# Optimization experiments

Hardware: AMD Instinct MI355X
Metric: run time of the kernel (lower is better)

## Reference

```python
import jax, jax.numpy as jnp
import numpy as np

TOP_K = 2
LORA_SCALE = 32.0 / 16.0  # alpha / r


def setup_inputs() -> dict:
    key = jax.random.key(0)
    ks = jax.random.split(key, 11)
    B, S, H, I, E, R = 4, 2048, 2048, 5504, 8, 16
    s = lambda k, shape, fan: jax.random.normal(k, shape, jnp.float32) / np.sqrt(fan)
    return {
        "x": jax.random.normal(ks[0], (B, S, H), jnp.float32),
        "gate_values": jax.random.normal(ks[1], (B, E), jnp.float32),
        "Wg": s(ks[2], (I, H), H),
        "Ag": s(ks[3], (E, H, R), H),
        "Bg": s(ks[4], (E, R, I), R),
        "Wu": s(ks[5], (I, H), H),
        "Au": s(ks[6], (E, H, R), H),
        "Bu": s(ks[7], (E, R, I), R),
        "Wd": s(ks[8], (H, I), I),
        "Ad": s(ks[9], (E, I, R), I),
        "Bd": s(ks[10], (E, R, H), R),
    }


def _top_k_binary_gates(gate_values, k):
    # set top-k entries per row to 1.0, others 0.0 (bsz, num_experts)
    _, idx = jax.lax.top_k(gate_values, k)
    b = jnp.zeros_like(gate_values)
    rows = jnp.arange(gate_values.shape[0])[:, None]
    return b.at[rows, idx].set(1.0)


def _adapter_linear(x, W, A, B, binary_gates):
    # base: (b,s,in) @ (out,in)^T -> (b,s,out)
    base = jnp.einsum("bsh,oh->bso", x, W)
    # per-expert LoRA: gate e * x @ A_e @ B_e, summed over selected experts
    u = jnp.einsum("bsh,ehr->bser", x, A)            # (b,s,E,r) low-rank
    delta = jnp.einsum("bser,ero,be->bso", u, B, binary_gates)
    return base + LORA_SCALE * delta


def reference(x, gate_values, Wg, Ag, Bg, Wu, Au, Bu, Wd, Ad, Bd):
    g = _top_k_binary_gates(gate_values, TOP_K)
    gate_out = _adapter_linear(x, Wg, Ag, Bg, g)
    up_out = _adapter_linear(x, Wu, Au, Bu, g)
    h = jax.nn.silu(gate_out) * up_out              # SwiGLU
    return _adapter_linear(h, Wd, Ad, Bd, g)
```

## Files before the change

### kernel.cpp

```cpp
#include <hip/hip_runtime.h>
#include <stdint.h>

typedef unsigned short u16;
typedef __bf16 bf16x8 __attribute__((ext_vector_type(8)));
typedef float f32x4 __attribute__((ext_vector_type(4)));

#define AS1 __attribute__((address_space(1)))
#define AS3 __attribute__((address_space(3)))

__device__ __forceinline__ void g2l16(const void* g, void* l) {
  __builtin_amdgcn_global_load_lds((AS1 void*)(void*)g, (AS3 void*)l, 16, 0, 0);
}

__device__ __forceinline__ u16 f2bf(float f) {
  union { float f; uint32_t u; } v; v.f = f;
  return (u16)((v.u + 0x7fffu + ((v.u >> 16) & 1u)) >> 16);
}
__device__ __forceinline__ float bf2f(u16 b) {
  union { uint32_t u; float f; } v; v.u = ((uint32_t)b) << 16;
  return v.f;
}

__global__ void k_cast4(const float* __restrict__ x, u16* __restrict__ xb,
                        const float* __restrict__ Wg, u16* __restrict__ Wgb,
                        const float* __restrict__ Wu, u16* __restrict__ Wub,
                        const float* __restrict__ Wd, u16* __restrict__ Wdb) {
  int i = blockIdx.x * 256 + threadIdx.x;
  const float* in; u16* out; int j;
  if (i < 4194304) { in = x; out = xb; j = i; }
  else if (i < 4194304 + 2818048) { in = Wg; out = Wgb; j = i - 4194304; }
  else if (i < 4194304 + 2 * 2818048) { in = Wu; out = Wub; j = i - 4194304 - 2818048; }
  else { in = Wd; out = Wdb; j = i - 4194304 - 2 * 2818048; }
  float4 v = ((const float4*)in)[j];
  ushort4 o = make_ushort4(f2bf(v.x), f2bf(v.y), f2bf(v.z), f2bf(v.w));
  ((ushort4*)out)[j] = o;
}

__global__ void k_prep(const float* __restrict__ gv,
                       const float* __restrict__ Ag, const float* __restrict__ Au,
                       const float* __restrict__ Ad,
                       const float* __restrict__ Bg, const float* __restrict__ Bu,
                       const float* __restrict__ Bd,
                       u16* __restrict__ AxT, u16* __restrict__ AdT,
                       u16* __restrict__ BgT, u16* __restrict__ BuT,
                       u16* __restrict__ BdT) {
  __shared__ int sidx[8];
  if (threadIdx.x == 0) {
    #pragma unroll
    for (int b = 0; b < 4; ++b) {
      const float* g = gv + b * 8;
      int i1 = 0; float v1 = g[0];
      for (int e = 1; e < 8; ++e) if (g[e] > v1) { v1 = g[e]; i1 = e; }
      int i2 = -1; float v2 = -3.0e38f;
      for (int e = 0; e < 8; ++e) if (e != i1 && g[e] > v2) { v2 = g[e]; i2 = e; }
      sidx[2 * b] = i1; sidx[2 * b + 1] = i2;
    }
  }
  __syncthreads();
  int t = blockIdx.x * 256 + threadIdx.x;
  if (t < 524288) {
    int h = t % 2048;
    int j = (t / 2048) & 63;
    int b = t / (2048 * 64);
    const float* src = (j >= 32) ? Au : Ag;
    int jj = j & 31;
    int e = sidx[2 * b + ((jj >> 4) & 1)];
    AxT[t] = f2bf(src[((size_t)e * 2048 + h) * 16 + (jj & 15)]);
    return;
  }
  t -= 524288;
  if (t < 704512) {
    int h = t % 5504;
    int j = (t / 5504) & 31;
    int b = t / (5504 * 32);
    int e = sidx[2 * b + ((j >> 4) & 1)];
    AdT[t] = f2bf(Ad[((size_t)e * 5504 + h) * 16 + (j & 15)]);
    return;
  }
  t -= 704512;
  if (t < 704512) {
    int j = t & 31;
    int n = (t >> 5) % 5504;
    int b = t / (5504 * 32);
    int e = (j & 16) ? sidx[2 * b + 1] : sidx[2 * b];
    BgT[t] = f2bf(Bg[((size_t)e * 16 + (j & 15)) * 5504 + n]);
    return;
  }
  t -= 704512;
  if (t < 704512) {
    int j = t & 31;
    int n = (t >> 5) % 5504;
    int b = t / (5504 * 32);
    int e = (j & 16) ? sidx[2 * b + 1] : sidx[2 * b];
    BuT[t] = f2bf(Bu[((size_t)e * 16 + (j & 15)) * 5504 + n]);
    return;
  }
  t -= 704512;
  if (t < 262144) {
    int j = t & 31;
    int n = (t >> 5) % 2048;
    int b = t / (2048 * 32);
    int e = (j & 16) ? sidx[2 * b + 1] : sidx[2 * b];
    BdT[t] = f2bf(Bd[((size_t)e * 16 + (j & 15)) * 2048 + n]);
  }
}

template <int N2>
__global__ __launch_bounds__(256) void k_skinny(
    const u16* __restrict__ A, const u16* __restrict__ BT,
    float* __restrict__ part, int M, int K, int total_iters, int iters_per_chunk) {
  __shared__ u16 sA[128 * 64];
  __shared__ u16 sB[N2 * 64];
  int nm = M >> 7;
  int bm = blockIdx.x % nm, chunk = blockIdx.x / nm;
  int m0 = bm << 7;
  int batch = m0 >> 11;
  int tid = threadIdx.x, lane = tid & 63, w = tid >> 6;
  int kb = chunk * iters_per_chunk;
  int ke = min(total_iters, kb + iters_per_chunk);

  const u16* Bb = BT + (size_t)batch * N2 * K;

  const u16* ga[4]; u16* la[4];
  #pragma unroll
  for (int t = 0; t < 4; ++t) {
    int cb = 4 * w + t;
    int q = cb * 64 + lane;
    int row = q >> 3;
    int c = (q & 7) ^ (row & 7);
    ga[t] = A + (size_t)(m0 + row) * K + (size_t)kb * 64 + c * 8;
    la[t] = sA + cb * 512;
  }
  constexpr int nB = N2 / 32;
  const u16* gb[nB]; u16* lb[nB];
  #pragma unroll
  for (int t = 0; t < nB; ++t) {
    int cb = nB * w + t;
    int q = cb * 64 + lane;
    int row = q >> 3;
    int c = (q & 7) ^ (row & 7);
    gb[t] = Bb + (size_t)row * K + (size_t)kb * 64 + c * 8;
    lb[t] = sB + cb * 512;
  }

  f32x4 acc[2][N2 / 16] = {};
  for (int kt = kb; kt < ke; ++kt) {
    #pragma unroll
    for (int t = 0; t < 4; ++t) { g2l16(ga[t], la[t]); ga[t] += 64; }
    #pragma unroll
    for (int t = 0; t < nB; ++t) { g2l16(gb[t], lb[t]); gb[t] += 64; }
    __syncthreads();
    #pragma unroll
    for (int ks = 0; ks < 2; ++ks) {
      int cb0 = ks * 4 + (lane >> 4);
      bf16x8 af[2], bfr[N2 / 16];
      #pragma unroll
      for (int mi = 0; mi < 2; ++mi) {
        int row = 32 * w + mi * 16 + (lane & 15);
        af[mi] = *(const bf16x8*)(sA + (row * 8 + (cb0 ^ (row & 7))) * 8);
      }
      #pragma unroll
      for (int ni = 0; ni < N2 / 16; ++ni) {
        int row = ni * 16 + (lane & 15);
        bfr[ni] = *(const bf16x8*)(sB + (row * 8 + (cb0 ^ (row & 7))) * 8);
      }
      #pragma unroll
      for (int mi = 0; mi < 2; ++mi)
        #pragma unroll
        for (int ni = 0; ni < N2 / 16; ++ni)
          acc[mi][ni] = __builtin_amdgcn_mfma_f32_16x16x32_bf16(
              af[mi], bfr[ni], acc[mi][ni], 0, 0, 0);
    }
    __syncthreads();
  }

  int rb = (lane >> 4) * 4, cc = lane & 15;
  #pragma unroll
  for (int mi = 0; mi < 2; ++mi)
    #pragma unroll
    for (int ni = 0; ni < N2 / 16; ++ni)
      #pragma unroll
      for (int reg = 0; reg < 4; ++reg) {
        int gr = m0 + 32 * w + mi * 16 + rb + reg;
        int gc = ni * 16 + cc;
        part[((size_t)chunk * M + gr) * N2 + gc] = acc[mi][ni][reg];
      }
}

__global__ void k_fin(const float* __restrict__ part, u16* __restrict__ out0,
                      u16* __restrict__ out1, int M, int N2, int nch) {
  int t = blockIdx.x * 256 + threadIdx.x;
  if (t >= M * N2) return;
  float s = 0.f;
  for (int c = 0; c < nch; ++c) s += part[(size_t)c * M * N2 + t];
  int j = t % N2, bs = t / N2;
  u16 v = f2bf(2.0f * s);
  if (N2 == 64) {
    if (j < 32) out0[(size_t)bs * 32 + j] = v;
    else        out1[(size_t)bs * 32 + (j - 32)] = v;
  } else {
    out0[(size_t)bs * 32 + j] = v;
  }
}

__global__ __launch_bounds__(256, 2)
void k_gemmGU(const u16* __restrict__ A, const u16* __restrict__ Bg_,
              const u16* __restrict__ Bu_,
              const u16* __restrict__ A2g, const u16* __restrict__ A2u,
              const u16* __restrict__ B2g, const u16* __restrict__ B2u,
              u16* __restrict__ Out, int N, int K) {
  __shared__ u16 sA[128 * 64];
  __shared__ u16 sG[128 * 64];
  __shared__ u16 sU[128 * 64];
  int nt = N >> 7;
  int nm = gridDim.x / nt;
  int perx = nm >> 3;
  int xcd = blockIdx.x & 7;
  int v = blockIdx.x >> 3;
  int bn = v / perx;
  int bm = xcd * perx + (v - bn * perx);
  int m0 = bm << 7, n0 = bn << 7;
  int tid = threadIdx.x, lane = tid & 63, w = tid >> 6;
  int mo = (w & 1) << 6, no = (w >> 1) << 6;

  const u16* ga[4]; const u16* gg[4]; const u16* gu[4];
  u16* la[4]; u16* lg[4]; u16* lu[4];
  #pragma unroll
  for (int t = 0; t < 4; ++t) {
    int cb = 4 * w + t;
    int q = cb * 64 + lane;
    int row = q >> 3;
    int c = (q & 7) ^ (row & 7);
    ga[t] = A + (size_t)(m0 + row) * K + c * 8;
    gg[t] = Bg_ + (size_t)(n0 + row) * K + c * 8;
    gu[t] = Bu_ + (size_t)(n0 + row) * K + c * 8;
    la[t] = sA + cb * 512;
    lg[t] = sG + cb * 512;
    lu[t] = sU + cb * 512;
  }

  f32x4 accg[4][4] = {};
  f32x4 accu[4][4] = {};

  int kiters = K >> 6;
  for (int kt = 0; kt < kiters; ++kt) {
    #pragma unroll
    for (int t = 0; t < 4; ++t) { g2l16(ga[t], la[t]); ga[t] += 64; }
    #pragma unroll
    for (int t = 0; t < 4; ++t) { g2l16(gg[t], lg[t]); gg[t] += 64; }
    #pragma unroll
    for (int t = 0; t < 4; ++t) { g2l16(gu[t], lu[t]); gu[t] += 64; }
    __syncthreads();
    #pragma unroll
    for (int ks = 0; ks < 2; ++ks) {
      bf16x8 af[4], bgf[4], buf_[4];
      int cb0 = ks * 4 + (lane >> 4);
      #pragma unroll
      for (int mi = 0; mi < 4; ++mi) {
        int row = mo + mi * 16 + (lane & 15);
        af[mi] = *(const bf16x8*)(sA + (row * 8 + (cb0 ^ (row & 7))) * 8);
      }
      #pragma unroll
      for (int ni = 0; ni < 4; ++ni) {
        int row = no + ni * 16 + (lane & 15);
        bgf[ni] = *(const bf16x8*)(sG + (row * 8 + (cb0 ^ (row & 7))) * 8);
        buf_[ni] = *(const bf16x8*)(sU + (row * 8 + (cb0 ^ (row & 7))) * 8);
      }
      #pragma unroll
      for (int mi = 0; mi < 4; ++mi)
        #pragma unroll
        for (int ni = 0; ni < 4; ++ni) {
          accg[mi][ni] = __builtin_amdgcn_mfma_f32_16x16x32_bf16(
              af[mi], bgf[ni], accg[mi][ni], 0, 0, 0);
          accu[mi][ni] = __builtin_amdgcn_mfma_f32_16x16x32_bf16(
              af[mi], buf_[ni], accu[mi][ni], 0, 0, 0);
        }
    }
    __syncthreads();
  }

  {
    int batch = m0 >> 11;
    const u16* B2gb = B2g + (size_t)batch * N * 32;
    const u16* B2ub = B2u + (size_t)batch * N * 32;
    #pragma unroll
    for (int t = 0; t < 2; ++t) {
      int cb = 2 * w + t;
      int q = cb * 64 + lane;
      int row = q >> 2;
      int c = (q & 3) ^ (row & 3);
      g2l16(A2g + (size_t)(m0 + row) * 32 + c * 8, sA + cb * 512);
      g2l16(A2u + (size_t)(m0 + row) * 32 + c * 8, sA + 4096 + cb * 512);
      g2l16(B2gb + (size_t)(n0 + row) * 32 + c * 8, sG + cb * 512);
      g2l16(B2ub + (size_t)(n0 + row) * 32 + c * 8, sU + cb * 512);
    }
    __syncthreads();
    int c0 = lane >> 4;
    bf16x8 ag2[4], au2[4], bg2[4], bu2[4];
    #pragma unroll
    for (int mi = 0; mi < 4; ++mi) {
      int row = mo + mi * 16 + (lane & 15);
      ag2[mi] = *(const bf16x8*)(sA + (row * 4 + (c0 ^ (row & 3))) * 8);
      au2[mi] = *(const bf16x8*)(sA + 4096 + (row * 4 + (c0 ^ (row & 3))) * 8);
    }
    #pragma unroll
    for (int ni = 0; ni < 4; ++ni) {
      int row = no + ni * 16 + (lane & 15);
      bg2[ni] = *(const bf16x8*)(sG + (row * 4 + (c0 ^ (row & 3))) * 8);
      bu2[ni] = *(const bf16x8*)(sU + (row * 4 + (c0 ^ (row & 3))) * 8);
    }
    #pragma unroll
    for (int mi = 0; mi < 4; ++mi)
      #pragma unroll
      for (int ni = 0; ni < 4; ++ni) {
        accg[mi][ni] = __builtin_amdgcn_mfma_f32_16x16x32_bf16(
            ag2[mi], bg2[ni], accg[mi][ni], 0, 0, 0);
        accu[mi][ni] = __builtin_amdgcn_mfma_f32_16x16x32_bf16(
            au2[mi], bu2[ni], accu[mi][ni], 0, 0, 0);
      }
  }

  int rb = (lane >> 4) * 4;
  int cc = lane & 15;
  #pragma unroll
  for (int mi = 0; mi < 4; ++mi) {
    #pragma unroll
    for (int ni = 0; ni < 4; ++ni) {
      #pragma unroll
      for (int reg = 0; reg < 4; ++reg) {
        int gr = m0 + mo + mi * 16 + rb + reg;
        int gc = n0 + no + ni * 16 + cc;
        size_t pos = (size_t)gr * N + gc;
        float gvv = accg[mi][ni][reg];
        float uvv = accu[mi][ni][reg];
        gvv = gvv / (1.f + __expf(-gvv));
        Out[pos] = f2bf(gvv * uvv);
      }
    }
  }
}

__global__ __launch_bounds__(256, 3)
void k_gemm(const u16* __restrict__ A, const u16* __restrict__ Bm,
            const u16* __restrict__ A2, const u16* __restrict__ B2,
            const u16* Gprev, void* Out,
            int N, int K, int mode) {
  __shared__ u16 sA[128 * 64];
  __shared__ u16 sB[128 * 64];
  int nt = N >> 7;
  int nm = gridDim.x / nt;
  int perx = nm >> 3;
  int xcd = blockIdx.x & 7;
  int v = blockIdx.x >> 3;
  int bn = v / perx;
  int bm = xcd * perx + (v - bn * perx);
  int m0 = bm << 7, n0 = bn << 7;
  int tid = threadIdx.x, lane = tid & 63, w = tid >> 6;
  int mo = (w & 1) << 6, no = (w >> 1) << 6;

  const u16* ga[4]; const u16* gb[4];
  u16* la[4]; u16* lb[4];
  #pragma unroll
  for (int t = 0; t < 4; ++t) {
    int cb = 4 * w + t;
    int q = cb * 64 + lane;
    int row = q >> 3;
    int c = (q & 7) ^ (row & 7);
    ga[t] = A + (size_t)(m0 + row) * K + c * 8;
    gb[t] = Bm + (size_t)(n0 + row) * K + c * 8;
    la[t] = sA + cb * 512;
    lb[t] = sB + cb * 512;
  }

  f32x4 acc[4][4] = {};

  int kiters = K >> 6;
  for (int kt = 0; kt < kiters; ++kt) {
    #pragma unroll
    for (int t = 0; t < 4; ++t) { g2l16(ga[t], la[t]); ga[t] += 64; }
    #pragma unroll
    for (int t = 0; t < 4; ++t) { g2l16(gb[t], lb[t]); gb[t] += 64; }
    __syncthreads();
    #pragma unroll
    for (int ks = 0; ks < 2; ++ks) {
      bf16x8 af[4], bfr[4];
      int cb0 = ks * 4 + (lane >> 4);
      #pragma unroll
      for (int mi = 0; mi < 4; ++mi) {
        int row = mo + mi * 16 + (lane & 15);
        af[mi] = *(const bf16x8*)(sA + (row * 8 + (cb0 ^ (row & 7))) * 8);
      }
      #pragma unroll
      for (int ni = 0; ni < 4; ++ni) {
        int row = no + ni * 16 + (lane & 15);
        bfr[ni] = *(const bf16x8*)(sB + (row * 8 + (cb0 ^ (row & 7))) * 8);
      }
      #pragma unroll
      for (int mi = 0; mi < 4; ++mi)
        #pragma unroll
        for (int ni = 0; ni < 4; ++ni)
          acc[mi][ni] = __builtin_amdgcn_mfma_f32_16x16x32_bf16(
              af[mi], bfr[ni], acc[mi][ni], 0, 0, 0);
    }
    __syncthreads();
  }

  {
    int batch = m0 >> 11;
    const u16* B2b = B2 + (size_t)batch * N * 32;
    #pragma unroll
    for (int t = 0; t < 2; ++t) {
      int cb = 2 * w + t;
      int q = cb * 64 + lane;
      int row = q >> 2;
      int c = (q & 3) ^ (row & 3);
      g2l16(A2 + (size_t)(m0 + row) * 32 + c * 8, sA + cb * 512);
      g2l16(B2b + (size_t)(n0 + row) * 32 + c * 8, sB + cb * 512);
    }
    __syncthreads();
    bf16x8 af[4], bfr[4];
    int c0 = lane >> 4;
    #pragma unroll
    for (int mi = 0; mi < 4; ++mi) {
      int row = mo + mi * 16 + (lane & 15);
      af[mi] = *(const bf16x8*)(sA + (row * 4 + (c0 ^ (row & 3))) * 8);
    }
    #pragma unroll
    for (int ni = 0; ni < 4; ++ni) {
      int row = no + ni * 16 + (lane & 15);
      bfr[ni] = *(const bf16x8*)(sB + (row * 4 + (c0 ^ (row & 3))) * 8);
    }
    #pragma unroll
    for (int mi = 0; mi < 4; ++mi)
      #pragma unroll
      for (int ni = 0; ni < 4; ++ni)
        acc[mi][ni] = __builtin_amdgcn_mfma_f32_16x16x32_bf16(
            af[mi], bfr[ni], acc[mi][ni], 0, 0, 0);
  }

  int rb = (lane >> 4) * 4;
  int cc = lane & 15;
  #pragma unroll
  for (int mi = 0; mi < 4; ++mi) {
    #pragma unroll
    for (int ni = 0; ni < 4; ++ni) {
      #pragma unroll
      for (int reg = 0; reg < 4; ++reg) {
        int gr = m0 + mo + mi * 16 + rb + reg;
        int gc = n0 + no + ni * 16 + cc;
        size_t pos = (size_t)gr * N + gc;
        float vv = acc[mi][ni][reg];
        if (mode == 0) {
          vv = vv / (1.f + __expf(-vv));
          ((u16*)Out)[pos] = f2bf(vv);
        } else if (mode == 1) {
          float gg = bf2f(Gprev[pos]);
          ((u16*)Out)[pos] = f2bf(gg * vv);
        } else {
          ((float*)Out)[pos] = vv;
        }
      }
    }
  }
}

extern "C" void kernel_launch(void* const* d_in, const int* in_sizes, int n_in,
                              void* d_out, int out_size, void* d_ws, size_t ws_size,
                              hipStream_t stream) {
  const float* x  = (const float*)d_in[0];
  const float* gv = (const float*)d_in[1];
  const float* Wg = (const float*)d_in[2];
  const float* Ag = (const float*)d_in[3];
  const float* Bg = (const float*)d_in[4];
  const float* Wu = (const float*)d_in[5];
  const float* Au = (const float*)d_in[6];
  const float* Bu = (const float*)d_in[7];
  const float* Wd = (const float*)d_in[8];
  const float* Ad = (const float*)d_in[9];
  const float* Bd = (const float*)d_in[10];
  float* out = (float*)d_out;

  char* ws = (char*)d_ws;
  size_t off = 0;
  auto alloc = [&](size_t bytes) -> void* {
    void* p = ws + off;
    off = (off + bytes + 255) & ~(size_t)255;
    return p;
  };
  u16* xb   = (u16*)alloc((size_t)8192 * 2048 * 2);
  u16* Wgb  = (u16*)alloc((size_t)5504 * 2048 * 2);
  u16* Wub  = (u16*)alloc((size_t)5504 * 2048 * 2);
  u16* Wdb  = (u16*)alloc((size_t)2048 * 5504 * 2);
  u16* xag  = (u16*)alloc((size_t)8192 * 32 * 2);
  u16* xau  = (u16*)alloc((size_t)8192 * 32 * 2);
  u16* ha   = (u16*)alloc((size_t)8192 * 32 * 2);
  u16* BgT  = (u16*)alloc((size_t)4 * 5504 * 32 * 2);
  u16* BuT  = (u16*)alloc((size_t)4 * 5504 * 32 * 2);
  u16* BdT  = (u16*)alloc((size_t)4 * 2048 * 32 * 2);
  u16* AxT  = (u16*)alloc((size_t)4 * 64 * 2048 * 2);
  u16* AdT  = (u16*)alloc((size_t)4 * 32 * 5504 * 2);
  u16* gbuf = (u16*)alloc((size_t)8192 * 5504 * 2);
  if (off > ws_size) return;

  float* part_xa = (float*)gbuf;
  float* part_ha = (float*)Wgb;

  k_cast4<<<49408, 256, 0, stream>>>(x, xb, Wg, Wgb, Wu, Wub, Wd, Wdb);
  k_prep<<<11328, 256, 0, stream>>>(gv, Ag, Au, Ad, Bg, Bu, Bd,
                                    AxT, AdT, BgT, BuT, BdT);

  k_skinny<64><<<64 * 16, 256, 0, stream>>>(xb, AxT, part_xa, 8192, 2048, 32, 2);
  k_fin<<<2048, 256, 0, stream>>>(part_xa, xag, xau, 8192, 64, 16);

  k_gemmGU<<<64 * 43, 256, 0, stream>>>(xb, Wgb, Wub, xag, xau, BgT, BuT,
                                        gbuf, 5504, 2048);

  k_skinny<32><<<64 * 16, 256, 0, stream>>>(gbuf, AdT, part_ha, 8192, 5504, 86, 6);
  k_fin<<<1024, 256, 0, stream>>>(part_ha, ha, ha, 8192, 32, 16);

  k_gemm<<<64 * 16, 256, 0, stream>>>(gbuf, Wdb, ha, BdT, (const u16*)nullptr,
                                      out, 2048, 5504, 2);
}
```

Measured before the change: 806.7 us.

## Fuse down-proj LoRA A product into gate/up GEMM epilogue; widen down GEMM tile

The gate/up GEMM epilogue now stages its SwiGLU output tile in shared memory and multiplies it by the selected-expert Ad slice, accumulating the low-rank h·Ad product into an fp32 buffer with atomics. This removes the separate skinny GEMM and its partial-sum reduction, which had to re-read the full 8192x5504 intermediate. The down GEMM is specialised into a 256x128 tile kernel, so each Wd tile is reused across two M blocks with fewer blocks launched. The cast and prep kernels are merged into one launch. The cost is extra shared-memory traffic and atomics in the gate/up epilogue, plus more accumulator registers in the down GEMM.

```diff
diff --git a/kernel.cpp b/kernel.cpp
--- a/kernel.cpp
+++ b/kernel.cpp
@@ -21,30 +21,31 @@
   return v.f;
 }
 
-__global__ void k_cast4(const float* __restrict__ x, u16* __restrict__ xb,
-                        const float* __restrict__ Wg, u16* __restrict__ Wgb,
-                        const float* __restrict__ Wu, u16* __restrict__ Wub,
-                        const float* __restrict__ Wd, u16* __restrict__ Wdb) {
-  int i = blockIdx.x * 256 + threadIdx.x;
-  const float* in; u16* out; int j;
-  if (i < 4194304) { in = x; out = xb; j = i; }
-  else if (i < 4194304 + 2818048) { in = Wg; out = Wgb; j = i - 4194304; }
-  else if (i < 4194304 + 2 * 2818048) { in = Wu; out = Wub; j = i - 4194304 - 2818048; }
-  else { in = Wd; out = Wdb; j = i - 4194304 - 2 * 2818048; }
-  float4 v = ((const float4*)in)[j];
-  ushort4 o = make_ushort4(f2bf(v.x), f2bf(v.y), f2bf(v.z), f2bf(v.w));
-  ((ushort4*)out)[j] = o;
-}
-
-__global__ void k_prep(const float* __restrict__ gv,
-                       const float* __restrict__ Ag, const float* __restrict__ Au,
-                       const float* __restrict__ Ad,
-                       const float* __restrict__ Bg, const float* __restrict__ Bu,
-                       const float* __restrict__ Bd,
-                       u16* __restrict__ AxT, u16* __restrict__ AdT,
-                       u16* __restrict__ BgT, u16* __restrict__ BuT,
-                       u16* __restrict__ BdT) {
+__global__ void k_pre(const float* __restrict__ x, u16* __restrict__ xb,
+                      const float* __restrict__ Wg, u16* __restrict__ Wgb,
+                      const float* __restrict__ Wu, u16* __restrict__ Wub,
+                      const float* __restrict__ Wd, u16* __restrict__ Wdb,
+                      const float* __restrict__ gv,
+                      const float* __restrict__ Ag, const float* __restrict__ Au,
+                      const float* __restrict__ Ad,
+                      const float* __restrict__ Bg, const float* __restrict__ Bu,
+                      const float* __restrict__ Bd,
+                      u16* __restrict__ AxT, u16* __restrict__ AdT,
+                      u16* __restrict__ BgT, u16* __restrict__ BuT,
+                      u16* __restrict__ BdT) {
   __shared__ int sidx[8];
+  if (blockIdx.x < 49408) {
+    int i = blockIdx.x * 256 + threadIdx.x;
+    const float* in; u16* out; int j;
+    if (i < 4194304) { in = x; out = xb; j = i; }
+    else if (i < 4194304 + 2818048) { in = Wg; out = Wgb; j = i - 4194304; }
+    else if (i < 4194304 + 2 * 2818048) { in = Wu; out = Wub; j = i - 4194304 - 2818048; }
+    else { in = Wd; out = Wdb; j = i - 4194304 - 2 * 2818048; }
+    float4 v = ((const float4*)in)[j];
+    ushort4 o = make_ushort4(f2bf(v.x), f2bf(v.y), f2bf(v.z), f2bf(v.w));
+    ((ushort4*)out)[j] = o;
+    return;
+  }
   if (threadIdx.x == 0) {
     #pragma unroll
     for (int b = 0; b < 4; ++b) {
@@ -57,7 +58,7 @@
     }
   }
   __syncthreads();
-  int t = blockIdx.x * 256 + threadIdx.x;
+  int t = (blockIdx.x - 49408) * 256 + threadIdx.x;
   if (t < 524288) {
     int h = t % 2048;
     int j = (t / 2048) & 63;
@@ -203,11 +204,17 @@
   }
 }
 
+__global__ void k_haf(const float* __restrict__ haf, u16* __restrict__ ha) {
+  int t = blockIdx.x * 256 + threadIdx.x;
+  if (t < 262144) ha[t] = f2bf(2.0f * haf[t]);
+}
+
 __global__ __launch_bounds__(256, 2)
 void k_gemmGU(const u16* __restrict__ A, const u16* __restrict__ Bg_,
               const u16* __restrict__ Bu_,
               const u16* __restrict__ A2g, const u16* __restrict__ A2u,
               const u16* __restrict__ B2g, const u16* __restrict__ B2u,
+              const u16* __restrict__ AdT, float* __restrict__ haf,
               u16* __restrict__ Out, int N, int K) {
   __shared__ u16 sA[128 * 64];
   __shared__ u16 sG[128 * 64];
@@ -220,6 +227,7 @@
   int bn = v / perx;
   int bm = xcd * perx + (v - bn * perx);
   int m0 = bm << 7, n0 = bn << 7;
+  int batch = m0 >> 11;
   int tid = threadIdx.x, lane = tid & 63, w = tid >> 6;
   int mo = (w & 1) << 6, no = (w >> 1) << 6;
 
@@ -280,7 +288,6 @@
   }
 
   {
-    int batch = m0 >> 11;
     const u16* B2gb = B2g + (size_t)batch * N * 32;
     const u16* B2ub = B2u + (size_t)batch * N * 32;
     #pragma unroll
@@ -320,6 +327,19 @@
       }
   }
 
+  __syncthreads();
+
+  {
+    const u16* AdTb = AdT + (size_t)batch * 32 * 5504;
+    int q = w * 64 + lane;
+    int row = q >> 3;
+    int c = (q & 7) ^ (row & 7);
+    #pragma unroll
+    for (int half = 0; half < 2; ++half)
+      g2l16(AdTb + (size_t)row * 5504 + n0 + half * 64 + c * 8,
+            sA + half * 2048 + w * 512);
+  }
+
   int rb = (lane >> 4) * 4;
   int cc = lane & 15;
   #pragma unroll
@@ -334,18 +354,63 @@
         float gvv = accg[mi][ni][reg];
         float uvv = accu[mi][ni][reg];
         gvv = gvv / (1.f + __expf(-gvv));
-        Out[pos] = f2bf(gvv * uvv);
-      }
-    }
-  }
-}
-
-__global__ __launch_bounds__(256, 3)
-void k_gemm(const u16* __restrict__ A, const u16* __restrict__ Bm,
-            const u16* __restrict__ A2, const u16* __restrict__ B2,
-            const u16* Gprev, void* Out,
-            int N, int K, int mode) {
-  __shared__ u16 sA[128 * 64];
+        u16 hv = f2bf(gvv * uvv);
+        Out[pos] = hv;
+        int cl = no + ni * 16 + cc;
+        u16* sH = (cl < 64) ? sG : sU;
+        int c2 = cl & 63;
+        int r2 = mo + mi * 16 + rb + reg;
+        sH[(r2 * 8 + ((c2 >> 3) ^ (r2 & 7))) * 8 + (c2 & 7)] = hv;
+      }
+    }
+  }
+  __syncthreads();
+
+  {
+    int moh = (w & 1) << 6;
+    int half = w >> 1;
+    const u16* sH = half ? sU : sG;
+    const u16* sAd = sA + half * 2048;
+    f32x4 ah[4][2] = {};
+    #pragma unroll
+    for (int ks = 0; ks < 2; ++ks) {
+      int cb0 = ks * 4 + (lane >> 4);
+      bf16x8 afh[4], bfh[2];
+      #pragma unroll
+      for (int mi = 0; mi < 4; ++mi) {
+        int row = moh + mi * 16 + (lane & 15);
+        afh[mi] = *(const bf16x8*)(sH + (row * 8 + (cb0 ^ (row & 7))) * 8);
+      }
+      #pragma unroll
+      for (int jf = 0; jf < 2; ++jf) {
+        int row = jf * 16 + (lane & 15);
+        bfh[jf] = *(const bf16x8*)(sAd + (row * 8 + (cb0 ^ (row & 7))) * 8);
+      }
+      #pragma unroll
+      for (int mi = 0; mi < 4; ++mi)
+        #pragma unroll
+        for (int jf = 0; jf < 2; ++jf)
+          ah[mi][jf] = __builtin_amdgcn_mfma_f32_16x16x32_bf16(
+              afh[mi], bfh[jf], ah[mi][jf], 0, 0, 0);
+    }
+    #pragma unroll
+    for (int mi = 0; mi < 4; ++mi)
+      #pragma unroll
+      for (int jf = 0; jf < 2; ++jf)
+        #pragma unroll
+        for (int reg = 0; reg < 4; ++reg)
+          atomicAdd(haf + (size_t)(m0 + moh + mi * 16 + rb + reg) * 32 +
+                        jf * 16 + cc,
+                    ah[mi][jf][reg]);
+  }
+}
+
+__global__ __launch_bounds__(256, 2)
+void k_gemmD(const u16* __restrict__ A, const u16* __restrict__ Bm,
+             const u16* __restrict__ A2, const u16* __restrict__ B2,
+             float* __restrict__ Out, int N, int K) {
+  __shared__ u16 sA0[128 * 64];
+  __shared__ u16 sA1[128 * 64];
   __shared__ u16 sB[128 * 64];
   int nt = N >> 7;
   int nm = gridDim.x / nt;
@@ -354,41 +419,48 @@
   int v = blockIdx.x >> 3;
   int bn = v / perx;
   int bm = xcd * perx + (v - bn * perx);
-  int m0 = bm << 7, n0 = bn << 7;
+  int m0 = bm << 8, n0 = bn << 7;
+  int batch = m0 >> 11;
   int tid = threadIdx.x, lane = tid & 63, w = tid >> 6;
   int mo = (w & 1) << 6, no = (w >> 1) << 6;
 
-  const u16* ga[4]; const u16* gb[4];
-  u16* la[4]; u16* lb[4];
+  const u16* ga0[4]; const u16* ga1[4]; const u16* gb[4];
+  u16* la0[4]; u16* la1[4]; u16* lb[4];
   #pragma unroll
   for (int t = 0; t < 4; ++t) {
     int cb = 4 * w + t;
     int q = cb * 64 + lane;
     int row = q >> 3;
     int c = (q & 7) ^ (row & 7);
-    ga[t] = A + (size_t)(m0 + row) * K + c * 8;
-    gb[t] = Bm + (size_t)(n0 + row) * K + c * 8;
-    la[t] = sA + cb * 512;
-    lb[t] = sB + cb * 512;
-  }
-
-  f32x4 acc[4][4] = {};
+    ga0[t] = A + (size_t)(m0 + row) * K + c * 8;
+    ga1[t] = A + (size_t)(m0 + 128 + row) * K + c * 8;
+    gb[t]  = Bm + (size_t)(n0 + row) * K + c * 8;
+    la0[t] = sA0 + cb * 512;
+    la1[t] = sA1 + cb * 512;
+    lb[t]  = sB + cb * 512;
+  }
+
+  f32x4 acc0[4][4] = {};
+  f32x4 acc1[4][4] = {};
 
   int kiters = K >> 6;
   for (int kt = 0; kt < kiters; ++kt) {
     #pragma unroll
-    for (int t = 0; t < 4; ++t) { g2l16(ga[t], la[t]); ga[t] += 64; }
+    for (int t = 0; t < 4; ++t) { g2l16(ga0[t], la0[t]); ga0[t] += 64; }
+    #pragma unroll
+    for (int t = 0; t < 4; ++t) { g2l16(ga1[t], la1[t]); ga1[t] += 64; }
     #pragma unroll
     for (int t = 0; t < 4; ++t) { g2l16(gb[t], lb[t]); gb[t] += 64; }
     __syncthreads();
     #pragma unroll
     for (int ks = 0; ks < 2; ++ks) {
-      bf16x8 af[4], bfr[4];
+      bf16x8 af0[4], af1[4], bfr[4];
       int cb0 = ks * 4 + (lane >> 4);
       #pragma unroll
       for (int mi = 0; mi < 4; ++mi) {
         int row = mo + mi * 16 + (lane & 15);
-        af[mi] = *(const bf16x8*)(sA + (row * 8 + (cb0 ^ (row & 7))) * 8);
+        af0[mi] = *(const bf16x8*)(sA0 + (row * 8 + (cb0 ^ (row & 7))) * 8);
+        af1[mi] = *(const bf16x8*)(sA1 + (row * 8 + (cb0 ^ (row & 7))) * 8);
       }
       #pragma unroll
       for (int ni = 0; ni < 4; ++ni) {
@@ -398,15 +470,17 @@
       #pragma unroll
       for (int mi = 0; mi < 4; ++mi)
         #pragma unroll
-        for (int ni = 0; ni < 4; ++ni)
-          acc[mi][ni] = __builtin_amdgcn_mfma_f32_16x16x32_bf16(
-              af[mi], bfr[ni], acc[mi][ni], 0, 0, 0);
+        for (int ni = 0; ni < 4; ++ni) {
+          acc0[mi][ni] = __builtin_amdgcn_mfma_f32_16x16x32_bf16(
+              af0[mi], bfr[ni], acc0[mi][ni], 0, 0, 0);
+          acc1[mi][ni] = __builtin_amdgcn_mfma_f32_16x16x32_bf16(
+              af1[mi], bfr[ni], acc1[mi][ni], 0, 0, 0);
+        }
     }
     __syncthreads();
   }
 
   {
-    int batch = m0 >> 11;
     const u16* B2b = B2 + (size_t)batch * N * 32;
     #pragma unroll
     for (int t = 0; t < 2; ++t) {
@@ -414,16 +488,18 @@
       int q = cb * 64 + lane;
       int row = q >> 2;
       int c = (q & 3) ^ (row & 3);
-      g2l16(A2 + (size_t)(m0 + row) * 32 + c * 8, sA + cb * 512);
+      g2l16(A2 + (size_t)(m0 + row) * 32 + c * 8, sA0 + cb * 512);
+      g2l16(A2 + (size_t)(m0 + 128 + row) * 32 + c * 8, sA1 + cb * 512);
       g2l16(B2b + (size_t)(n0 + row) * 32 + c * 8, sB + cb * 512);
     }
     __syncthreads();
-    bf16x8 af[4], bfr[4];
     int c0 = lane >> 4;
+    bf16x8 af0[4], af1[4], bfr[4];
     #pragma unroll
     for (int mi = 0; mi < 4; ++mi) {
       int row = mo + mi * 16 + (lane & 15);
-      af[mi] = *(const bf16x8*)(sA + (row * 4 + (c0 ^ (row & 3))) * 8);
+      af0[mi] = *(const bf16x8*)(sA0 + (row * 4 + (c0 ^ (row & 3))) * 8);
+      af1[mi] = *(const bf16x8*)(sA1 + (row * 4 + (c0 ^ (row & 3))) * 8);
     }
     #pragma unroll
     for (int ni = 0; ni < 4; ++ni) {
@@ -433,9 +509,12 @@
     #pragma unroll
     for (int mi = 0; mi < 4; ++mi)
       #pragma unroll
-      for (int ni = 0; ni < 4; ++ni)
-        acc[mi][ni] = __builtin_amdgcn_mfma_f32_16x16x32_bf16(
-            af[mi], bfr[ni], acc[mi][ni], 0, 0, 0);
+      for (int ni = 0; ni < 4; ++ni) {
+        acc0[mi][ni] = __builtin_amdgcn_mfma_f32_16x16x32_bf16(
+            af0[mi], bfr[ni], acc0[mi][ni], 0, 0, 0);
+        acc1[mi][ni] = __builtin_amdgcn_mfma_f32_16x16x32_bf16(
+            af1[mi], bfr[ni], acc1[mi][ni], 0, 0, 0);
+      }
   }
 
   int rb = (lane >> 4) * 4;
@@ -448,17 +527,8 @@
       for (int reg = 0; reg < 4; ++reg) {
         int gr = m0 + mo + mi * 16 + rb + reg;
         int gc = n0 + no + ni * 16 + cc;
-        size_t pos = (size_t)gr * N + gc;
-        float vv = acc[mi][ni][reg];
-        if (mode == 0) {
-          vv = vv / (1.f + __expf(-vv));
-          ((u16*)Out)[pos] = f2bf(vv);
-        } else if (mode == 1) {
-          float gg = bf2f(Gprev[pos]);
-          ((u16*)Out)[pos] = f2bf(gg * vv);
-        } else {
-          ((float*)Out)[pos] = vv;
-        }
+        Out[(size_t)gr * N + gc] = acc0[mi][ni][reg];
+        Out[(size_t)(gr + 128) * N + gc] = acc1[mi][ni][reg];
       }
     }
   }
@@ -499,25 +569,25 @@
   u16* BdT  = (u16*)alloc((size_t)4 * 2048 * 32 * 2);
   u16* AxT  = (u16*)alloc((size_t)4 * 64 * 2048 * 2);
   u16* AdT  = (u16*)alloc((size_t)4 * 32 * 5504 * 2);
+  float* haf = (float*)alloc((size_t)8192 * 32 * 4);
   u16* gbuf = (u16*)alloc((size_t)8192 * 5504 * 2);
   if (off > ws_size) return;
 
   float* part_xa = (float*)gbuf;
-  float* part_ha = (float*)Wgb;
-
-  k_cast4<<<49408, 256, 0, stream>>>(x, xb, Wg, Wgb, Wu, Wub, Wd, Wdb);
-  k_prep<<<11328, 256, 0, stream>>>(gv, Ag, Au, Ad, Bg, Bu, Bd,
-                                    AxT, AdT, BgT, BuT, BdT);
+
+  hipMemsetAsync(haf, 0, (size_t)8192 * 32 * 4, stream);
+
+  k_pre<<<60736, 256, 0, stream>>>(x, xb, Wg, Wgb, Wu, Wub, Wd, Wdb,
+                                   gv, Ag, Au, Ad, Bg, Bu, Bd,
+                                   AxT, AdT, BgT, BuT, BdT);
 
   k_skinny<64><<<64 * 16, 256, 0, stream>>>(xb, AxT, part_xa, 8192, 2048, 32, 2);
   k_fin<<<2048, 256, 0, stream>>>(part_xa, xag, xau, 8192, 64, 16);
 
   k_gemmGU<<<64 * 43, 256, 0, stream>>>(xb, Wgb, Wub, xag, xau, BgT, BuT,
-                                        gbuf, 5504, 2048);
-
-  k_skinny<32><<<64 * 16, 256, 0, stream>>>(gbuf, AdT, part_ha, 8192, 5504, 86, 6);
-  k_fin<<<1024, 256, 0, stream>>>(part_ha, ha, ha, 8192, 32, 16);
-
-  k_gemm<<<64 * 16, 256, 0, stream>>>(gbuf, Wdb, ha, BdT, (const u16*)nullptr,
-                                      out, 2048, 5504, 2);
-}
+                                        AdT, haf, gbuf, 5504, 2048);
+
+  k_haf<<<1024, 256, 0, stream>>>(haf, ha);
+
+  k_gemmD<<<32 * 16, 256, 0, stream>>>(gbuf, Wdb, ha, BdT, out, 2048, 5504);
+}
```

After: 785.8 us. 2.6% less time.
